# Kernel optimization log

Hardware: AMD Instinct MI355X
Metric: run time of the kernel (lower is better)

The kernel has to match this reference:

```python
import jax, jax.numpy as jnp
import numpy as np

WS = 8; SHIFT = 4; HEADS = 6
B = 2; H0 = 256; W0 = 256; C0 = 192; HID = 768; RED = 8


def _rel_pos_index(ws):
    coords = np.stack(np.meshgrid(np.arange(ws), np.arange(ws), indexing='ij')).reshape(2, -1)
    rel = (coords[:, :, None] - coords[:, None, :]).transpose(1, 2, 0)
    rel[:, :, 0] += ws - 1
    rel[:, :, 1] += ws - 1
    rel[:, :, 0] *= 2 * ws - 1
    return rel.sum(-1)  # (N, N) int


def _attn_mask(H, W, ws, shift):
    # exact translation of SwinTransformerBlock.calculate_mask (static, numpy)
    img = np.zeros((H, W))
    sl = (slice(0, -ws), slice(-ws, -shift), slice(-shift, None))
    cnt = 0
    for hs in sl:
        for wsl in sl:
            img[hs, wsl] = cnt
            cnt += 1
    mw = img.reshape(H // ws, ws, W // ws, ws).transpose(0, 2, 1, 3).reshape(-1, ws * ws)
    am = mw[:, None, :] - mw[:, :, None]  # (nW, N, N)
    return jnp.asarray(np.where(am != 0, -100.0, 0.0).astype(np.float32))


def _ln(x, g, b, eps=1e-5):
    m = x.mean(-1, keepdims=True)
    v = ((x - m) ** 2).mean(-1, keepdims=True)
    return (x - m) * jax.lax.rsqrt(v + eps) * g + b


def setup_inputs():
    key = jax.random.key(0)
    ks = jax.random.split(key, 12)
    C = C0
    r = C // RED
    def nrm(k, shape, std=0.02):
        return jax.random.normal(k, shape, dtype=jnp.float32) * std
    return {
        'x': jax.random.normal(ks[0], (B, H0 * W0, C), dtype=jnp.float32),
        'norm1_g': jnp.ones((C,), jnp.float32),
        'norm1_b': jnp.zeros((C,), jnp.float32),
        'qkv_w': nrm(ks[1], (3 * C, C)),
        'qkv_b': jnp.zeros((3 * C,), jnp.float32),
        'rpb_table': nrm(ks[2], ((2 * WS - 1) ** 2, HEADS)),
        'proj_w': nrm(ks[3], (C, C)),
        'proj_b': jnp.zeros((C,), jnp.float32),
        'norm2_g': jnp.ones((C,), jnp.float32),
        'norm2_b': jnp.zeros((C,), jnp.float32),
        'fc1_w': nrm(ks[4], (HID, C)),
        'fc1_b': jnp.zeros((HID,), jnp.float32),
        'fc2_w': nrm(ks[5], (C, HID)),
        'fc2_b': jnp.zeros((C,), jnp.float32),
        'lce_c1_w': nrm(ks[6], (r, C, 1, 1)),
        'lce_c1_b': jnp.zeros((r,), jnp.float32),
        'lce_c2_w': nrm(ks[7], (r, r, 3, 3)),
        'lce_c2_b': jnp.zeros((r,), jnp.float32),
        'lce_c3_w': nrm(ks[8], (C, r, 1, 1)),
        'lce_c3_b': jnp.zeros((C,), jnp.float32),
        'lce_fc1_w': nrm(ks[9], (r, C)),
        'lce_fc2_w': nrm(ks[10], (C, r)),
        'H': H0,
        'W': W0,
    }


def reference(x, norm1_g, norm1_b, qkv_w, qkv_b, rpb_table, proj_w, proj_b,
              norm2_g, norm2_b, fc1_w, fc1_b, fc2_w, fc2_b,
              lce_c1_w, lce_c1_b, lce_c2_w, lce_c2_b, lce_c3_w, lce_c3_b,
              lce_fc1_w, lce_fc2_w, H, W):
    Bs, L, C = x.shape
    ws, shift, nh = WS, SHIFT, HEADS
    hd = C // nh
    N = ws * ws
    shortcut = x
    xn = _ln(x, norm1_g, norm1_b).reshape(Bs, H, W, C)
    lcf = xn.transpose(0, 3, 1, 2)  # (B, C, H, W) local-context input
    # cyclic shift + window partition
    sx = jnp.roll(xn, (-shift, -shift), axis=(1, 2))
    nWh, nWw = H // ws, W // ws
    xw = sx.reshape(Bs, nWh, ws, nWw, ws, C).transpose(0, 1, 3, 2, 4, 5).reshape(-1, N, C)
    Bn = xw.shape[0]
    # W-MSA with relative position bias
    qkv = (xw @ qkv_w.T + qkv_b).reshape(Bn, N, 3, nh, hd).transpose(2, 0, 3, 1, 4)
    q, k, v = qkv[0], qkv[1], qkv[2]
    attn = jnp.einsum('bhnd,bhmd->bhnm', q * (hd ** -0.5), k)
    rpi = _rel_pos_index(ws)
    bias = rpb_table[rpi.reshape(-1)].reshape(N, N, nh).transpose(2, 0, 1)  # (nh, N, N)
    attn = attn + bias[None]
    mask = _attn_mask(H, W, ws, shift)  # (nW, N, N)
    nW = mask.shape[0]
    attn = (attn.reshape(Bs, nW, nh, N, N) + mask[None, :, None]).reshape(Bn, nh, N, N)
    attn = jax.nn.softmax(attn, axis=-1)
    out = jnp.einsum('bhnm,bhmd->bhnd', attn, v).transpose(0, 2, 1, 3).reshape(Bn, N, C)
    out = out @ proj_w.T + proj_b
    # window reverse + reverse shift
    sx = out.reshape(Bs, nWh, nWw, ws, ws, C).transpose(0, 1, 3, 2, 4, 5).reshape(Bs, H, W, C)
    xa = jnp.roll(sx, (shift, shift), axis=(1, 2)).reshape(Bs, H * W, C)
    x1 = shortcut + xa
    # MLP (exact GELU, matches torch default)
    h = _ln(x1, norm2_g, norm2_b)
    h = jax.nn.gelu(h @ fc1_w.T + fc1_b, approximate=False)
    x2 = x1 + (h @ fc2_w.T + fc2_b)
    # LocalContextExtractor: conv1x1 -> conv3x3 -> conv1x1 -> LeakyReLU(0.2) -> SE gate
    dn = ('NCHW', 'OIHW', 'NCHW')
    y = jax.lax.conv_general_dilated(lcf, lce_c1_w, (1, 1), 'VALID', dimension_numbers=dn) + lce_c1_b[None, :, None, None]
    y = jax.lax.conv_general_dilated(y, lce_c2_w, (1, 1), [(1, 1), (1, 1)], dimension_numbers=dn) + lce_c2_b[None, :, None, None]
    y = jax.lax.conv_general_dilated(y, lce_c3_w, (1, 1), 'VALID', dimension_numbers=dn) + lce_c3_b[None, :, None, None]
    y = jnp.where(y >= 0, y, 0.2 * y)
    s = y.mean((2, 3))  # (B, C) global avg pool
    s = jax.nn.sigmoid(jax.nn.relu(s @ lce_fc1_w.T) @ lce_fc2_w.T)
    lc = y * s[:, :, None, None]
    lc = lc.reshape(Bs, C, H * W).transpose(0, 2, 1)
    return lc + x2
```

## Files before the change

### kernel.cpp

```cpp
#include <hip/hip_runtime.h>
#include <hip/hip_bf16.h>

using bf16 = __hip_bfloat16;
typedef __attribute__((ext_vector_type(8))) short short8;
typedef __attribute__((ext_vector_type(4))) float float4v;

constexpr int NTOK = 131072;

constexpr size_t OFF_T1   = 50331648;
constexpr size_t OFF_T2   = 62914560;
constexpr size_t OFF_S0   = 75497472;
constexpr size_t OFF_WQKV = 75500544;
constexpr size_t OFF_WPRJ = 75721728;
constexpr size_t OFF_WFC1 = 75795456;
constexpr size_t OFF_WFC2 = 76090368;
constexpr size_t OFF_C1WB = 76385280;
constexpr size_t WS_NEEDED = 76397568;

__device__ __forceinline__ int region256(int t) { return t < 248 ? 0 : (t < 252 ? 1 : 2); }

__device__ __forceinline__ short8 lds8(const bf16* p) {
  return *reinterpret_cast<const short8*>(p);
}
__device__ __forceinline__ short8 glb8(const bf16* p) {
  return *reinterpret_cast<const short8*>(p);
}

__global__ __launch_bounds__(256) void k_f2b_all(const float* __restrict__ qkvw, const float* __restrict__ projw,
                                                 const float* __restrict__ w1, const float* __restrict__ w2,
                                                 const float* __restrict__ c1w,
                                                 bf16* __restrict__ wqkv, bf16* __restrict__ wprj,
                                                 bf16* __restrict__ wfc1, bf16* __restrict__ wfc2,
                                                 bf16* __restrict__ c1wb, float* __restrict__ s0) {
  int i = blockIdx.x * 256 + threadIdx.x;
  if (i < 110592) { wqkv[i] = __float2bfloat16(qkvw[i]); return; }
  i -= 110592;
  if (i < 36864) { wprj[i] = __float2bfloat16(projw[i]); return; }
  i -= 36864;
  if (i < 147456) { wfc1[i] = __float2bfloat16(w1[i]); return; }
  i -= 147456;
  if (i < 147456) { wfc2[i] = __float2bfloat16(w2[i]); return; }
  i -= 147456;
  if (i < 4608) { c1wb[i] = __float2bfloat16(c1w[i]); return; }
  i -= 4608;
  if (i < 1536) { c1wb[4608 + i] = __float2bfloat16(0.f); return; }
  i -= 1536;
  if (i < 384) s0[i] = 0.f;
}

__device__ __forceinline__ int stg_b(int r, int c) { return (r * 384 + c * 2) ^ ((r & 7) << 4); }
__device__ __forceinline__ int kl1_b(int r, int c) { return 24576 + ((r * 64 + c * 2) ^ ((r & 7) << 4)); }
__device__ __forceinline__ int vt1_b(int r, int c) { return 28672 + ((r * 128 + c * 2) ^ ((r & 7) << 4)); }
__device__ __forceinline__ int ps3_b(int r, int c) { return 32768 + ((r * 128 + c * 2) ^ ((r & 7) << 4)); }

__device__ __forceinline__ short8 lds8o(const char* sm, int byteoff) {
  return *reinterpret_cast<const short8*>(sm + byteoff);
}
__device__ __forceinline__ void st16(char* sm, int byteoff, bf16 v) {
  *reinterpret_cast<bf16*>(sm + byteoff) = v;
}

__global__ __launch_bounds__(256, 3) void k_attn2(const float* __restrict__ x, const float* __restrict__ g,
                                                  const float* __restrict__ bb, const bf16* __restrict__ wq,
                                                  const float* __restrict__ qkvb, const float* __restrict__ rpb,
                                                  const bf16* __restrict__ wp, const float* __restrict__ projb,
                                                  const bf16* __restrict__ c1wb, const float* __restrict__ c1b,
                                                  float* __restrict__ t1, float* __restrict__ x1out) {
  __shared__ char sm[40960];

  int win = blockIdx.x;
  int b = win >> 10;
  int wrem = win & 1023;
  int wh = wrem >> 5, ww = wrem & 31;
  int tid = threadIdx.x;
  int wave = tid >> 6, lane = tid & 63;
  int colB = lane & 15, grp = lane >> 4;
  const float scale = 0.17677669529663687f;

  for (int t = 0; t < 16; ++t) {
    int tok = wave * 16 + t;
    int i = tok >> 3, j = tok & 7;
    int hp = (wh * 8 + i + 4) & 255;
    int wpp = (ww * 8 + j + 4) & 255;
    const float* xr = x + (((size_t)b << 16) + (hp << 8) + wpp) * 192;
    float v0 = xr[lane], v1 = xr[lane + 64], v2 = xr[lane + 128];
    float s = v0 + v1 + v2;
    for (int o = 32; o > 0; o >>= 1) s += __shfl_down(s, o);
    s = __shfl(s, 0);
    float m = s * (1.f / 192.f);
    float d0 = v0 - m, d1 = v1 - m, d2 = v2 - m;
    float q = d0 * d0 + d1 * d1 + d2 * d2;
    for (int o = 32; o > 0; o >>= 1) q += __shfl_down(q, o);
    q = __shfl(q, 0);
    float inv = rsqrtf(q * (1.f / 192.f) + 1e-5f);
    st16(sm, stg_b(tok, lane),       __float2bfloat16(d0 * inv * g[lane]       + bb[lane]));
    st16(sm, stg_b(tok, lane + 64),  __float2bfloat16(d1 * inv * g[lane + 64]  + bb[lane + 64]));
    st16(sm, stg_b(tok, lane + 128), __float2bfloat16(d2 * inv * g[lane + 128] + bb[lane + 128]));
  }

  short8 axw[6];
#pragma unroll
  for (int kk = 0; kk < 6; ++kk) axw[kk] = lds8o(sm, stg_b(wave * 16 + colB, kk * 32 + 8 * grp));

  int l1r[4], i1r[4], j1r[4];
#pragma unroll
  for (int r = 0; r < 4; ++r) {
    int n = wave * 16 + 4 * grp + r;
    i1r[r] = n >> 3; j1r[r] = n & 7;
    l1r[r] = region256(wh * 8 + i1r[r]) * 3 + region256(ww * 8 + j1r[r]);
  }

  for (int gch = 0; gch < 6; ++gch) {
    float qreg[8];
    {
      float4v qa[2] = {{0,0,0,0},{0,0,0,0}};
      short8 wf[6];
#pragma unroll
      for (int h2 = 0; h2 < 2; ++h2) {
#pragma unroll
        for (int kk = 0; kk < 3; ++kk)
#pragma unroll
          for (int jt = 0; jt < 2; ++jt)
            wf[kk * 2 + jt] = glb8(wq + (size_t)(gch * 32 + jt * 16 + colB) * 192 + (h2 * 3 + kk) * 32 + 8 * grp);
#pragma unroll
        for (int kk = 0; kk < 3; ++kk)
#pragma unroll
          for (int jt = 0; jt < 2; ++jt)
            qa[jt] = __builtin_amdgcn_mfma_f32_16x16x32_bf16(axw[h2 * 3 + kk], wf[kk * 2 + jt], qa[jt], 0, 0, 0);
      }
#pragma unroll
      for (int jt = 0; jt < 2; ++jt) {
        float bias = qkvb[gch * 32 + jt * 16 + colB];
#pragma unroll
        for (int r = 0; r < 4; ++r) qreg[jt * 4 + r] = (qa[jt][r] + bias) * scale;
      }
    }
    {
      float4v ka[2] = {{0,0,0,0},{0,0,0,0}};
      short8 wf[6];
#pragma unroll
      for (int h2 = 0; h2 < 2; ++h2) {
#pragma unroll
        for (int kk = 0; kk < 3; ++kk)
#pragma unroll
          for (int jt = 0; jt < 2; ++jt)
            wf[kk * 2 + jt] = glb8(wq + (size_t)(192 + gch * 32 + jt * 16 + colB) * 192 + (h2 * 3 + kk) * 32 + 8 * grp);
#pragma unroll
        for (int kk = 0; kk < 3; ++kk)
#pragma unroll
          for (int jt = 0; jt < 2; ++jt)
            ka[jt] = __builtin_amdgcn_mfma_f32_16x16x32_bf16(axw[h2 * 3 + kk], wf[kk * 2 + jt], ka[jt], 0, 0, 0);
      }
#pragma unroll
      for (int jt = 0; jt < 2; ++jt) {
        float bias = qkvb[192 + gch * 32 + jt * 16 + colB];
#pragma unroll
        for (int r = 0; r < 4; ++r)
          st16(sm, kl1_b(wave * 16 + 4 * grp + r, jt * 16 + colB), __float2bfloat16(ka[jt][r] + bias));
      }
    }
    {
      float4v va[2] = {{0,0,0,0},{0,0,0,0}};
      short8 wf[6];
#pragma unroll
      for (int h2 = 0; h2 < 2; ++h2) {
#pragma unroll
        for (int kk = 0; kk < 3; ++kk)
#pragma unroll
          for (int jt = 0; jt < 2; ++jt)
            wf[kk * 2 + jt] = glb8(wq + (size_t)(384 + gch * 32 + jt * 16 + colB) * 192 + (h2 * 3 + kk) * 32 + 8 * grp);
#pragma unroll
        for (int kk = 0; kk < 3; ++kk)
#pragma unroll
          for (int jt = 0; jt < 2; ++jt)
            va[jt] = __builtin_amdgcn_mfma_f32_16x16x32_bf16(axw[h2 * 3 + kk], wf[kk * 2 + jt], va[jt], 0, 0, 0);
      }
#pragma unroll
      for (int jt = 0; jt < 2; ++jt) {
        float bias = qkvb[384 + gch * 32 + jt * 16 + colB];
#pragma unroll
        for (int r = 0; r < 4; ++r)
          st16(sm, vt1_b(jt * 16 + colB, wave * 16 + 4 * grp + r), __float2bfloat16(va[jt][r] + bias));
      }
    }
    if (gch == 0) {
      float4v acc[2] = {{0,0,0,0},{0,0,0,0}};
      short8 wf[6];
#pragma unroll
      for (int h2 = 0; h2 < 2; ++h2) {
#pragma unroll
        for (int kk = 0; kk < 3; ++kk)
#pragma unroll
          for (int j = 0; j < 2; ++j)
            wf[kk * 2 + j] = glb8(c1wb + (size_t)(j * 16 + colB) * 192 + (h2 * 3 + kk) * 32 + 8 * grp);
#pragma unroll
        for (int kk = 0; kk < 3; ++kk)
#pragma unroll
          for (int j = 0; j < 2; ++j)
            acc[j] = __builtin_amdgcn_mfma_f32_16x16x32_bf16(axw[h2 * 3 + kk], wf[kk * 2 + j], acc[j], 0, 0, 0);
      }
#pragma unroll
      for (int j = 0; j < 2; ++j) {
        int ch = j * 16 + colB;
        if (ch < 24) {
          float bias = c1b[ch];
#pragma unroll
          for (int r = 0; r < 4; ++r) {
            int tok = wave * 16 + 4 * grp + r;
            int i = tok >> 3, jj = tok & 7;
            int hp = (wh * 8 + i + 4) & 255;
            int wpp = (ww * 8 + jj + 4) & 255;
            size_t pix = ((size_t)b << 16) + (hp << 8) + wpp;
            t1[pix * 24 + ch] = acc[j][r] + bias;
          }
        }
      }
    }
    __syncthreads();

    {
      int h = gch;
#pragma unroll
      for (int t = 0; t < 2; ++t)
#pragma unroll
        for (int r = 0; r < 4; ++r)
          st16(sm, ps3_b(wave * 16 + 4 * grp + r, t * 16 + colB), __float2bfloat16(qreg[t * 4 + r]));
      short8 aq = lds8o(sm, ps3_b(wave * 16 + colB, 8 * grp));

      float4v s[4];
#pragma unroll
      for (int nt = 0; nt < 4; ++nt) {
        short8 bk = lds8o(sm, kl1_b(nt * 16 + colB, 8 * grp));
        float4v z = {0, 0, 0, 0};
        s[nt] = __builtin_amdgcn_mfma_f32_16x16x32_bf16(aq, bk, z, 0, 0, 0);
      }
#pragma unroll
      for (int nt = 0; nt < 4; ++nt) {
        int m = nt * 16 + colB;
        int i2 = m >> 3, j2 = m & 7;
        int l2 = region256(wh * 8 + i2) * 3 + region256(ww * 8 + j2);
#pragma unroll
        for (int r = 0; r < 4; ++r) {
          float bias = rpb[((i1r[r] - i2 + 7) * 15 + (j1r[r] - j2 + 7)) * 6 + h];
          s[nt][r] += bias + (l1r[r] != l2 ? -100.f : 0.f);
        }
      }
#pragma unroll
      for (int r = 0; r < 4; ++r) {
        float mx = fmaxf(fmaxf(s[0][r], s[1][r]), fmaxf(s[2][r], s[3][r]));
        mx = fmaxf(mx, __shfl_xor(mx, 1));
        mx = fmaxf(mx, __shfl_xor(mx, 2));
        mx = fmaxf(mx, __shfl_xor(mx, 4));
        mx = fmaxf(mx, __shfl_xor(mx, 8));
        float e0 = __expf(s[0][r] - mx), e1 = __expf(s[1][r] - mx);
        float e2 = __expf(s[2][r] - mx), e3 = __expf(s[3][r] - mx);
        float sum = e0 + e1 + e2 + e3;
        sum += __shfl_xor(sum, 1);
        sum += __shfl_xor(sum, 2);
        sum += __shfl_xor(sum, 4);
        sum += __shfl_xor(sum, 8);
        float inv = 1.f / sum;
        int row = wave * 16 + 4 * grp + r;
        st16(sm, ps3_b(row, 0 * 16 + colB), __float2bfloat16(e0 * inv));
        st16(sm, ps3_b(row, 1 * 16 + colB), __float2bfloat16(e1 * inv));
        st16(sm, ps3_b(row, 2 * 16 + colB), __float2bfloat16(e2 * inv));
        st16(sm, ps3_b(row, 3 * 16 + colB), __float2bfloat16(e3 * inv));
      }
      short8 ap0 = lds8o(sm, ps3_b(wave * 16 + colB, 8 * grp));
      short8 ap1 = lds8o(sm, ps3_b(wave * 16 + colB, 32 + 8 * grp));

      float4v o0 = {0, 0, 0, 0}, o1 = {0, 0, 0, 0};
      o0 = __builtin_amdgcn_mfma_f32_16x16x32_bf16(ap0, lds8o(sm, vt1_b(colB, 8 * grp)), o0, 0, 0, 0);
      o0 = __builtin_amdgcn_mfma_f32_16x16x32_bf16(ap1, lds8o(sm, vt1_b(colB, 32 + 8 * grp)), o0, 0, 0, 0);
      o1 = __builtin_amdgcn_mfma_f32_16x16x32_bf16(ap0, lds8o(sm, vt1_b(16 + colB, 8 * grp)), o1, 0, 0, 0);
      o1 = __builtin_amdgcn_mfma_f32_16x16x32_bf16(ap1, lds8o(sm, vt1_b(16 + colB, 32 + 8 * grp)), o1, 0, 0, 0);
      int ocol = gch * 32;
#pragma unroll
      for (int r = 0; r < 4; ++r) {
        int row = wave * 16 + 4 * grp + r;
        st16(sm, stg_b(row, ocol + colB),      __float2bfloat16(o0[r]));
        st16(sm, stg_b(row, ocol + 16 + colB), __float2bfloat16(o1[r]));
      }
    }
    if (gch != 5) __syncthreads();
  }

  short8 ao[6];
#pragma unroll
  for (int kk = 0; kk < 6; ++kk) ao[kk] = lds8o(sm, stg_b(wave * 16 + colB, kk * 32 + 8 * grp));
  for (int gp = 0; gp < 4; ++gp) {
    float4v acc[3] = {{0,0,0,0},{0,0,0,0},{0,0,0,0}};
#pragma unroll
    for (int half = 0; half < 2; ++half) {
      short8 wfp[9];
#pragma unroll
      for (int kk = 0; kk < 3; ++kk)
#pragma unroll
        for (int j = 0; j < 3; ++j)
          wfp[kk * 3 + j] = glb8(wp + (size_t)((gp * 3 + j) * 16 + colB) * 192 + (half * 3 + kk) * 32 + 8 * grp);
#pragma unroll
      for (int kk = 0; kk < 3; ++kk)
#pragma unroll
        for (int j = 0; j < 3; ++j)
          acc[j] = __builtin_amdgcn_mfma_f32_16x16x32_bf16(ao[half * 3 + kk], wfp[kk * 3 + j], acc[j], 0, 0, 0);
    }
#pragma unroll
    for (int j = 0; j < 3; ++j) {
      int col = (gp * 3 + j) * 16 + colB;
      float bias = projb[col];
#pragma unroll
      for (int r = 0; r < 4; ++r) {
        int n = wave * 16 + 4 * grp + r;
        int i = n >> 3, jj = n & 7;
        int hd2 = (wh * 8 + i + 4) & 255;
        int wd2 = (ww * 8 + jj + 4) & 255;
        size_t p = (((size_t)b << 16) + (hd2 << 8) + wd2) * 192 + col;
        x1out[p] = x[p] + acc[j][r] + bias;
      }
    }
  }
}

__global__ __launch_bounds__(256, 2) void k_mlp_lce2(float* __restrict__ x1, const float* __restrict__ g,
                                                     const float* __restrict__ bb, const bf16* __restrict__ w1,
                                                     const float* __restrict__ b1, const bf16* __restrict__ w2,
                                                     const float* __restrict__ b2,
                                                     const float* __restrict__ t1, const float* __restrict__ cw,
                                                     const float* __restrict__ cbia, float* __restrict__ t2,
                                                     const float* __restrict__ c3w, const float* __restrict__ c3b,
                                                     float* __restrict__ s0) {
  extern __shared__ __align__(16) char smu[];
  int tid = threadIdx.x;

  if (blockIdx.x < 512) {
    float* halo = (float*)smu;
    float* wlds = (float*)(smu + 32400);
    int bid = blockIdx.x;
    int b = bid >> 8;
    int rem = bid & 255;
    int ty0 = ((rem >> 4) & 15) * 16, tx0 = (rem & 15) * 16;
    for (int idx = tid; idx < 5184; idx += 256) wlds[idx] = cw[idx];
    for (int idx = tid; idx < 18 * 18 * 24; idx += 256) {
      int ch = idx % 24;
      int pp = idx / 24;
      int hy = pp / 18, hx = pp - hy * 18;
      int gy = ty0 + hy - 1, gx = tx0 + hx - 1;
      float v = 0.f;
      if (gy >= 0 && gy < 256 && gx >= 0 && gx < 256)
        v = t1[((size_t)(b << 16) + (gy << 8) + gx) * 24 + ch];
      halo[pp * 25 + ch] = v;
    }
    __syncthreads();
    int py = tid >> 4, px = tid & 15;
    float acc[24];
#pragma unroll
    for (int ro = 0; ro < 24; ++ro) acc[ro] = cbia[ro];
    for (int ky = 0; ky < 3; ++ky) {
      for (int kx = 0; kx < 3; ++kx) {
        int base = ((py + ky) * 18 + px + kx) * 25;
        float inb[24];
#pragma unroll
        for (int ri = 0; ri < 24; ++ri) inb[ri] = halo[base + ri];
        int wo = ky * 3 + kx;
#pragma unroll
        for (int ro = 0; ro < 24; ++ro) {
          float a = acc[ro];
#pragma unroll
          for (int ri = 0; ri < 24; ++ri) a += inb[ri] * wlds[ro * 216 + ri * 9 + wo];
          acc[ro] = a;
        }
      }
    }
    size_t pix = (size_t)(b << 16) + ((ty0 + py) << 8) + tx0 + px;
#pragma unroll
    for (int ro = 0; ro < 24; ++ro) t2[pix * 24 + ro] = acc[ro];

    __syncthreads();
    float* t2l = (float*)smu;
#pragma unroll
    for (int ro = 0; ro < 24; ++ro) t2l[tid * 28 + ro] = acc[ro];
    __syncthreads();
    if (tid < 192) {
      float wr3[24];
#pragma unroll
      for (int i2 = 0; i2 < 24; ++i2) wr3[i2] = c3w[tid * 24 + i2];
      float b3 = c3b[tid];
      float ps = 0.f;
      for (int p = 0; p < 256; ++p) {
        const float4v* rp = reinterpret_cast<const float4v*>(&t2l[p * 28]);
        float a = b3;
#pragma unroll
        for (int v = 0; v < 6; ++v) {
          float4v q = rp[v];
          a += q[0] * wr3[v * 4] + q[1] * wr3[v * 4 + 1] + q[2] * wr3[v * 4 + 2] + q[3] * wr3[v * 4 + 3];
        }
        ps += (a < 0.f) ? 0.2f * a : a;
      }
      atomicAdd(&s0[b * 192 + tid], ps);
    }
    return;
  }

  bf16 (*xl)[200] = reinterpret_cast<bf16(*)[200]>(smu);
  bf16 (*hh)[392] = reinterpret_cast<bf16(*)[392]>(smu + 25600);
  int wave = tid >> 6, lane = tid & 63;
  int colB = lane & 15, grp = lane >> 4;
  size_t tokbase = (size_t)(blockIdx.x - 512) * 64;

  for (int t = wave; t < 64; t += 4) {
    const float* xr = x1 + (tokbase + t) * 192;
    float v0 = xr[lane], v1 = xr[lane + 64], v2 = xr[lane + 128];
    float s = v0 + v1 + v2;
    for (int o = 32; o > 0; o >>= 1) s += __shfl_down(s, o);
    s = __shfl(s, 0);
    float m = s * (1.f / 192.f);
    float d0 = v0 - m, d1 = v1 - m, d2 = v2 - m;
    float qq = d0 * d0 + d1 * d1 + d2 * d2;
    for (int o = 32; o > 0; o >>= 1) qq += __shfl_down(qq, o);
    qq = __shfl(qq, 0);
    float inv = rsqrtf(qq * (1.f / 192.f) + 1e-5f);
    xl[t][lane]       = __float2bfloat16(d0 * inv * g[lane]       + bb[lane]);
    xl[t][lane + 64]  = __float2bfloat16(d1 * inv * g[lane + 64]  + bb[lane + 64]);
    xl[t][lane + 128] = __float2bfloat16(d2 * inv * g[lane + 128] + bb[lane + 128]);
  }
  __syncthreads();

  short8 a1f[6][2];
#pragma unroll
  for (int kk = 0; kk < 6; ++kk) {
    a1f[kk][0] = lds8(&xl[colB][kk * 32 + 8 * grp]);
    a1f[kk][1] = lds8(&xl[16 + colB][kk * 32 + 8 * grp]);
  }

  float4v d[3][4];
#pragma unroll
  for (int j = 0; j < 3; ++j)
#pragma unroll
    for (int tt = 0; tt < 4; ++tt) d[j][tt] = (float4v){0, 0, 0, 0};
  int ntb = wave * 3;

  for (int ph = 0; ph < 2; ++ph) {
    if (ph) __syncthreads();
    for (int nn = 0; nn < 6; ++nn) {
      int ntl = wave * 6 + nn;
      int colg = ph * 384 + ntl * 16 + colB;
      short8 wf1[6];
#pragma unroll
      for (int kk = 0; kk < 6; ++kk)
        wf1[kk] = glb8(w1 + (size_t)colg * 192 + kk * 32 + 8 * grp);
      float4v c0 = {0,0,0,0}, c1 = {0,0,0,0}, c2 = {0,0,0,0}, c3 = {0,0,0,0};
#pragma unroll
      for (int kk = 0; kk < 6; ++kk) {
        c0 = __builtin_amdgcn_mfma_f32_16x16x32_bf16(a1f[kk][0], wf1[kk], c0, 0, 0, 0);
        c1 = __builtin_amdgcn_mfma_f32_16x16x32_bf16(a1f[kk][1], wf1[kk], c1, 0, 0, 0);
        c2 = __builtin_amdgcn_mfma_f32_16x16x32_bf16(lds8(&xl[32 + colB][kk * 32 + 8 * grp]), wf1[kk], c2, 0, 0, 0);
        c3 = __builtin_amdgcn_mfma_f32_16x16x32_bf16(lds8(&xl[48 + colB][kk * 32 + 8 * grp]), wf1[kk], c3, 0, 0, 0);
      }
      float bias = b1[colg];
      int coll = ntl * 16 + colB;
#pragma unroll
      for (int r = 0; r < 4; ++r) {
        float v0 = c0[r] + bias;
        float v1 = c1[r] + bias;
        float v2 = c2[r] + bias;
        float v3 = c3[r] + bias;
        v0 = v0 * 0.5f * (1.f + erff(v0 * 0.70710678118654752f));
        v1 = v1 * 0.5f * (1.f + erff(v1 * 0.70710678118654752f));
        v2 = v2 * 0.5f * (1.f + erff(v2 * 0.70710678118654752f));
        v3 = v3 * 0.5f * (1.f + erff(v3 * 0.70710678118654752f));
        hh[4 * grp + r][coll]      = __float2bfloat16(v0);
        hh[16 + 4 * grp + r][coll] = __float2bfloat16(v1);
        hh[32 + 4 * grp + r][coll] = __float2bfloat16(v2);
        hh[48 + 4 * grp + r][coll] = __float2bfloat16(v3);
      }
    }
    __syncthreads();
    for (int kk = 0; kk < 12; ++kk) {
      int kol = kk * 32 + 8 * grp;
      int kog = ph * 384 + kol;
      short8 wf2[3];
#pragma unroll
      for (int j = 0; j < 3; ++j)
        wf2[j] = glb8(w2 + (size_t)((ntb + j) * 16 + colB) * 768 + kog);
      short8 h0 = lds8(&hh[colB][kol]);
      short8 h1 = lds8(&hh[16 + colB][kol]);
      short8 h2 = lds8(&hh[32 + colB][kol]);
      short8 h3 = lds8(&hh[48 + colB][kol]);
#pragma unroll
      for (int j = 0; j < 3; ++j) {
        d[j][0] = __builtin_amdgcn_mfma_f32_16x16x32_bf16(h0, wf2[j], d[j][0], 0, 0, 0);
        d[j][1] = __builtin_amdgcn_mfma_f32_16x16x32_bf16(h1, wf2[j], d[j][1], 0, 0, 0);
        d[j][2] = __builtin_amdgcn_mfma_f32_16x16x32_bf16(h2, wf2[j], d[j][2], 0, 0, 0);
        d[j][3] = __builtin_amdgcn_mfma_f32_16x16x32_bf16(h3, wf2[j], d[j][3], 0, 0, 0);
      }
    }
  }

#pragma unroll
  for (int j = 0; j < 3; ++j) {
    int col = (ntb + j) * 16 + colB;
    float bias = b2[col];
#pragma unroll
    for (int tt = 0; tt < 4; ++tt) {
#pragma unroll
      for (int r = 0; r < 4; ++r) {
        size_t p = (tokbase + tt * 16 + 4 * grp + r) * 192 + col;
        x1[p] += d[j][tt][r] + bias;
      }
    }
  }
}

__global__ __launch_bounds__(192) void k_final3(float* __restrict__ out, const float* __restrict__ t2,
                                                const float* __restrict__ c3w, const float* __restrict__ c3b,
                                                const float* __restrict__ s0, const float* __restrict__ w1se,
                                                const float* __restrict__ w2se) {
  __shared__ float mean[192];
  __shared__ float tt[24];
  __shared__ __align__(16) float t2l[64 * 24];
  int b = blockIdx.x >> 10;
  int chunk = blockIdx.x & 1023;
  int tid = threadIdx.x;
  mean[tid] = s0[b * 192 + tid] * (1.f / 65536.f);
  size_t pix0 = (size_t)b * 65536 + chunk * 64;
  for (int idx = tid; idx < 1536; idx += 192) t2l[idx] = t2[pix0 * 24 + idx];
  __syncthreads();
  if (tid < 24) {
    float a = 0.f;
    for (int c = 0; c < 192; ++c) a += mean[c] * w1se[tid * 192 + c];
    tt[tid] = fmaxf(a, 0.f);
  }
  __syncthreads();
  float a = 0.f;
#pragma unroll
  for (int r = 0; r < 24; ++r) a += tt[r] * w2se[tid * 24 + r];
  float gate = 1.f / (1.f + expf(-a));

  float wr3[24];
#pragma unroll
  for (int i = 0; i < 24; ++i) wr3[i] = c3w[tid * 24 + i];
  float b3 = c3b[tid];
  for (int p = 0; p < 64; ++p) {
    const float4v* rp = reinterpret_cast<const float4v*>(&t2l[p * 24]);
    float acc = b3;
#pragma unroll
    for (int v = 0; v < 6; ++v) {
      float4v q = rp[v];
      acc += q[0] * wr3[v * 4] + q[1] * wr3[v * 4 + 1] + q[2] * wr3[v * 4 + 2] + q[3] * wr3[v * 4 + 3];
    }
    if (acc < 0.f) acc *= 0.2f;
    out[(pix0 + p) * 192 + tid] += acc * gate;
  }
}

extern "C" void kernel_launch(void* const* d_in, const int* in_sizes, int n_in,
                              void* d_out, int out_size, void* d_ws, size_t ws_size,
                              hipStream_t stream) {
  const float* x     = (const float*)d_in[0];
  const float* n1g   = (const float*)d_in[1];
  const float* n1b   = (const float*)d_in[2];
  const float* qkvw  = (const float*)d_in[3];
  const float* qkvb  = (const float*)d_in[4];
  const float* rpb   = (const float*)d_in[5];
  const float* projw = (const float*)d_in[6];
  const float* projb = (const float*)d_in[7];
  const float* n2g   = (const float*)d_in[8];
  const float* n2b   = (const float*)d_in[9];
  const float* w1    = (const float*)d_in[10];
  const float* b1    = (const float*)d_in[11];
  const float* w2    = (const float*)d_in[12];
  const float* b2    = (const float*)d_in[13];
  const float* c1w   = (const float*)d_in[14];
  const float* c1b   = (const float*)d_in[15];
  const float* c2w   = (const float*)d_in[16];
  const float* c2b   = (const float*)d_in[17];
  const float* c3w   = (const float*)d_in[18];
  const float* c3b   = (const float*)d_in[19];
  const float* sfc1  = (const float*)d_in[20];
  const float* sfc2  = (const float*)d_in[21];
  float* out = (float*)d_out;

  if (ws_size < WS_NEEDED) return;

  char* ws = (char*)d_ws;
  float* t1   = (float*)(ws + OFF_T1);
  float* t2   = (float*)(ws + OFF_T2);
  float* s0   = (float*)(ws + OFF_S0);
  bf16*  wqkv = (bf16*)(ws + OFF_WQKV);
  bf16*  wprj = (bf16*)(ws + OFF_WPRJ);
  bf16*  wfc1 = (bf16*)(ws + OFF_WFC1);
  bf16*  wfc2 = (bf16*)(ws + OFF_WFC2);
  bf16*  c1wb = (bf16*)(ws + OFF_C1WB);

  hipFuncSetAttribute((const void*)k_mlp_lce2, hipFuncAttributeMaxDynamicSharedMemorySize, 75776);

  k_f2b_all<<<1754, 256, 0, stream>>>(qkvw, projw, w1, w2, c1w,
                                      wqkv, wprj, wfc1, wfc2, c1wb, s0);

  k_attn2<<<2048, 256, 0, stream>>>(x, n1g, n1b, wqkv, qkvb, rpb, wprj, projb,
                                    c1wb, c1b, t1, out);
  k_mlp_lce2<<<2560, 256, 75776, stream>>>(out, n2g, n2b, wfc1, b1, wfc2, b2,
                                           t1, c2w, c2b, t2, c3w, c3b, s0);
  k_final3<<<2048, 192, 0, stream>>>(out, t2, c3w, c3b, s0, sfc1, sfc2);
}
```

Baseline: 885.2 us.

## Process two adjacent windows per attention block to reuse weight fragments

```diff
diff --git a/kernel.cpp b/kernel.cpp
--- a/kernel.cpp
+++ b/kernel.cpp
@@ -49,9 +49,9 @@
 }
 
 __device__ __forceinline__ int stg_b(int r, int c) { return (r * 384 + c * 2) ^ ((r & 7) << 4); }
-__device__ __forceinline__ int kl1_b(int r, int c) { return 24576 + ((r * 64 + c * 2) ^ ((r & 7) << 4)); }
-__device__ __forceinline__ int vt1_b(int r, int c) { return 28672 + ((r * 128 + c * 2) ^ ((r & 7) << 4)); }
-__device__ __forceinline__ int ps3_b(int r, int c) { return 32768 + ((r * 128 + c * 2) ^ ((r & 7) << 4)); }
+__device__ __forceinline__ int kl1_b(int r, int c) { return 49152 + ((r * 64 + c * 2) ^ ((r & 7) << 4)); }
+__device__ __forceinline__ int vt1_b(int r, int c) { return 57344 + ((r * 256 + c * 2) ^ ((r & 7) << 4)); }
+__device__ __forceinline__ int ps3_b(int r, int c) { return 65536 + ((r * 128 + c * 2) ^ ((r & 7) << 4)); }
 
 __device__ __forceinline__ short8 lds8o(const char* sm, int byteoff) {
   return *reinterpret_cast<const short8*>(sm + byteoff);
@@ -60,60 +60,73 @@
   *reinterpret_cast<bf16*>(sm + byteoff) = v;
 }
 
-__global__ __launch_bounds__(256, 3) void k_attn2(const float* __restrict__ x, const float* __restrict__ g,
+constexpr int SMEM_ATTN = 73728;
+
+__global__ __launch_bounds__(256, 2) void k_attn2(const float* __restrict__ x, const float* __restrict__ g,
                                                   const float* __restrict__ bb, const bf16* __restrict__ wq,
                                                   const float* __restrict__ qkvb, const float* __restrict__ rpb,
                                                   const bf16* __restrict__ wp, const float* __restrict__ projb,
                                                   const bf16* __restrict__ c1wb, const float* __restrict__ c1b,
                                                   float* __restrict__ t1, float* __restrict__ x1out) {
-  __shared__ char sm[40960];
-
-  int win = blockIdx.x;
-  int b = win >> 10;
-  int wrem = win & 1023;
-  int wh = wrem >> 5, ww = wrem & 31;
+  extern __shared__ char sm[];
+
+  int pb = blockIdx.x;
+  int b = pb >> 9;
+  int rem = pb & 511;
+  int wh = rem >> 4, pw = rem & 15;
+  int ww0 = pw << 1;
   int tid = threadIdx.x;
   int wave = tid >> 6, lane = tid & 63;
   int colB = lane & 15, grp = lane >> 4;
   const float scale = 0.17677669529663687f;
 
-  for (int t = 0; t < 16; ++t) {
-    int tok = wave * 16 + t;
-    int i = tok >> 3, j = tok & 7;
-    int hp = (wh * 8 + i + 4) & 255;
-    int wpp = (ww * 8 + j + 4) & 255;
-    const float* xr = x + (((size_t)b << 16) + (hp << 8) + wpp) * 192;
-    float v0 = xr[lane], v1 = xr[lane + 64], v2 = xr[lane + 128];
-    float s = v0 + v1 + v2;
-    for (int o = 32; o > 0; o >>= 1) s += __shfl_down(s, o);
-    s = __shfl(s, 0);
-    float m = s * (1.f / 192.f);
-    float d0 = v0 - m, d1 = v1 - m, d2 = v2 - m;
-    float q = d0 * d0 + d1 * d1 + d2 * d2;
-    for (int o = 32; o > 0; o >>= 1) q += __shfl_down(q, o);
-    q = __shfl(q, 0);
-    float inv = rsqrtf(q * (1.f / 192.f) + 1e-5f);
-    st16(sm, stg_b(tok, lane),       __float2bfloat16(d0 * inv * g[lane]       + bb[lane]));
-    st16(sm, stg_b(tok, lane + 64),  __float2bfloat16(d1 * inv * g[lane + 64]  + bb[lane + 64]));
-    st16(sm, stg_b(tok, lane + 128), __float2bfloat16(d2 * inv * g[lane + 128] + bb[lane + 128]));
-  }
-
-  short8 axw[6];
-#pragma unroll
-  for (int kk = 0; kk < 6; ++kk) axw[kk] = lds8o(sm, stg_b(wave * 16 + colB, kk * 32 + 8 * grp));
-
-  int l1r[4], i1r[4], j1r[4];
+#pragma unroll
+  for (int wn = 0; wn < 2; ++wn) {
+    int wwc = ww0 + wn;
+    for (int t = 0; t < 16; ++t) {
+      int tok = wave * 16 + t;
+      int i = tok >> 3, j = tok & 7;
+      int hp = (wh * 8 + i + 4) & 255;
+      int wpp = (wwc * 8 + j + 4) & 255;
+      const float* xr = x + (((size_t)b << 16) + (hp << 8) + wpp) * 192;
+      float v0 = xr[lane], v1 = xr[lane + 64], v2 = xr[lane + 128];
+      float s = v0 + v1 + v2;
+      for (int o = 32; o > 0; o >>= 1) s += __shfl_down(s, o);
+      s = __shfl(s, 0);
+      float m = s * (1.f / 192.f);
+      float d0 = v0 - m, d1 = v1 - m, d2 = v2 - m;
+      float q = d0 * d0 + d1 * d1 + d2 * d2;
+      for (int o = 32; o > 0; o >>= 1) q += __shfl_down(q, o);
+      q = __shfl(q, 0);
+      float inv = rsqrtf(q * (1.f / 192.f) + 1e-5f);
+      int sr = wn * 64 + tok;
+      st16(sm, stg_b(sr, lane),       __float2bfloat16(d0 * inv * g[lane]       + bb[lane]));
+      st16(sm, stg_b(sr, lane + 64),  __float2bfloat16(d1 * inv * g[lane + 64]  + bb[lane + 64]));
+      st16(sm, stg_b(sr, lane + 128), __float2bfloat16(d2 * inv * g[lane + 128] + bb[lane + 128]));
+    }
+  }
+
+  short8 axwA[6], axwB[6];
+#pragma unroll
+  for (int kk = 0; kk < 6; ++kk) {
+    axwA[kk] = lds8o(sm, stg_b(wave * 16 + colB, kk * 32 + 8 * grp));
+    axwB[kk] = lds8o(sm, stg_b(64 + wave * 16 + colB, kk * 32 + 8 * grp));
+  }
+
+  int i1r[4], j1r[4], l1rA[4], l1rB[4];
 #pragma unroll
   for (int r = 0; r < 4; ++r) {
     int n = wave * 16 + 4 * grp + r;
     i1r[r] = n >> 3; j1r[r] = n & 7;
-    l1r[r] = region256(wh * 8 + i1r[r]) * 3 + region256(ww * 8 + j1r[r]);
+    int rh = region256(wh * 8 + i1r[r]) * 3;
+    l1rA[r] = rh + region256(ww0 * 8 + j1r[r]);
+    l1rB[r] = rh + region256((ww0 + 1) * 8 + j1r[r]);
   }
 
   for (int gch = 0; gch < 6; ++gch) {
-    float qreg[8];
+    float qreg[16];
     {
-      float4v qa[2] = {{0,0,0,0},{0,0,0,0}};
+      float4v qa[4] = {{0,0,0,0},{0,0,0,0},{0,0,0,0},{0,0,0,0}};
       short8 wf[6];
 #pragma unroll
       for (int h2 = 0; h2 < 2; ++h2) {
@@ -125,18 +138,23 @@
 #pragma unroll
         for (int kk = 0; kk < 3; ++kk)
 #pragma unroll
-          for (int jt = 0; jt < 2; ++jt)
-            qa[jt] = __builtin_amdgcn_mfma_f32_16x16x32_bf16(axw[h2 * 3 + kk], wf[kk * 2 + jt], qa[jt], 0, 0, 0);
+          for (int jt = 0; jt < 2; ++jt) {
+            qa[jt]     = __builtin_amdgcn_mfma_f32_16x16x32_bf16(axwA[h2 * 3 + kk], wf[kk * 2 + jt], qa[jt], 0, 0, 0);
+            qa[2 + jt] = __builtin_amdgcn_mfma_f32_16x16x32_bf16(axwB[h2 * 3 + kk], wf[kk * 2 + jt], qa[2 + jt], 0, 0, 0);
+          }
       }
 #pragma unroll
       for (int jt = 0; jt < 2; ++jt) {
         float bias = qkvb[gch * 32 + jt * 16 + colB];
 #pragma unroll
-        for (int r = 0; r < 4; ++r) qreg[jt * 4 + r] = (qa[jt][r] + bias) * scale;
+        for (int r = 0; r < 4; ++r) {
+          qreg[jt * 4 + r]     = (qa[jt][r] + bias) * scale;
+          qreg[8 + jt * 4 + r] = (qa[2 + jt][r] + bias) * scale;
+        }
       }
     }
     {
-      float4v ka[2] = {{0,0,0,0},{0,0,0,0}};
+      float4v ka[4] = {{0,0,0,0},{0,0,0,0},{0,0,0,0},{0,0,0,0}};
       short8 wf[6];
 #pragma unroll
       for (int h2 = 0; h2 < 2; ++h2) {
@@ -148,19 +166,23 @@
 #pragma unroll
         for (int kk = 0; kk < 3; ++kk)
 #pragma unroll
-          for (int jt = 0; jt < 2; ++jt)
-            ka[jt] = __builtin_amdgcn_mfma_f32_16x16x32_bf16(axw[h2 * 3 + kk], wf[kk * 2 + jt], ka[jt], 0, 0, 0);
+          for (int jt = 0; jt < 2; ++jt) {
+            ka[jt]     = __builtin_amdgcn_mfma_f32_16x16x32_bf16(axwA[h2 * 3 + kk], wf[kk * 2 + jt], ka[jt], 0, 0, 0);
+            ka[2 + jt] = __builtin_amdgcn_mfma_f32_16x16x32_bf16(axwB[h2 * 3 + kk], wf[kk * 2 + jt], ka[2 + jt], 0, 0, 0);
+          }
       }
 #pragma unroll
       for (int jt = 0; jt < 2; ++jt) {
         float bias = qkvb[192 + gch * 32 + jt * 16 + colB];
 #pragma unroll
-        for (int r = 0; r < 4; ++r)
+        for (int r = 0; r < 4; ++r) {
           st16(sm, kl1_b(wave * 16 + 4 * grp + r, jt * 16 + colB), __float2bfloat16(ka[jt][r] + bias));
+          st16(sm, kl1_b(64 + wave * 16 + 4 * grp + r, jt * 16 + colB), __float2bfloat16(ka[2 + jt][r] + bias));
+        }
       }
     }
     {
-      float4v va[2] = {{0,0,0,0},{0,0,0,0}};
+      float4v va[4] = {{0,0,0,0},{0,0,0,0},{0,0,0,0},{0,0,0,0}};
       short8 wf[6];
 #pragma unroll
       for (int h2 = 0; h2 < 2; ++h2) {
@@ -172,19 +194,24 @@
 #pragma unroll
         for (int kk = 0; kk < 3; ++kk)
 #pragma unroll
-          for (int jt = 0; jt < 2; ++jt)
-            va[jt] = __builtin_amdgcn_mfma_f32_16x16x32_bf16(axw[h2 * 3 + kk], wf[kk * 2 + jt], va[jt], 0, 0, 0);
+          for (int jt = 0; jt < 2; ++jt) {
+            va[jt]     = __builtin_amdgcn_mfma_f32_16x16x32_bf16(axwA[h2 * 3 + kk], wf[kk * 2 + jt], va[jt], 0, 0, 0);
+            va[2 + jt] = __builtin_amdgcn_mfma_f32_16x16x32_bf16(axwB[h2 * 3 + kk], wf[kk * 2 + jt], va[2 + jt], 0, 0, 0);
+          }
       }
 #pragma unroll
       for (int jt = 0; jt < 2; ++jt) {
         float bias = qkvb[384 + gch * 32 + jt * 16 + colB];
 #pragma unroll
-        for (int r = 0; r < 4; ++r)
+        for (int r = 0; r < 4; ++r) {
           st16(sm, vt1_b(jt * 16 + colB, wave * 16 + 4 * grp + r), __float2bfloat16(va[jt][r] + bias));
+          st16(sm, vt1_b(jt * 16 + colB, 64 + wave * 16 + 4 * grp + r), __float2bfloat16(va[2 + jt][r] + bias));
+        }
       }
     }
     if (gch == 0) {
-      float4v acc[2] = {{0,0,0,0},{0,0,0,0}};
+      float4v accA[2] = {{0,0,0,0},{0,0,0,0}};
+      float4v accB[2] = {{0,0,0,0},{0,0,0,0}};
       short8 wf[6];
 #pragma unroll
       for (int h2 = 0; h2 < 2; ++h2) {
@@ -196,8 +223,10 @@
 #pragma unroll
         for (int kk = 0; kk < 3; ++kk)
 #pragma unroll
-          for (int j = 0; j < 2; ++j)
-            acc[j] = __builtin_amdgcn_mfma_f32_16x16x32_bf16(axw[h2 * 3 + kk], wf[kk * 2 + j], acc[j], 0, 0, 0);
+          for (int j = 0; j < 2; ++j) {
+            accA[j] = __builtin_amdgcn_mfma_f32_16x16x32_bf16(axwA[h2 * 3 + kk], wf[kk * 2 + j], accA[j], 0, 0, 0);
+            accB[j] = __builtin_amdgcn_mfma_f32_16x16x32_bf16(axwB[h2 * 3 + kk], wf[kk * 2 + j], accB[j], 0, 0, 0);
+          }
       }
 #pragma unroll
       for (int j = 0; j < 2; ++j) {
@@ -209,28 +238,31 @@
             int tok = wave * 16 + 4 * grp + r;
             int i = tok >> 3, jj = tok & 7;
             int hp = (wh * 8 + i + 4) & 255;
-            int wpp = (ww * 8 + jj + 4) & 255;
-            size_t pix = ((size_t)b << 16) + (hp << 8) + wpp;
-            t1[pix * 24 + ch] = acc[j][r] + bias;
+            int wppA = (ww0 * 8 + jj + 4) & 255;
+            int wppB = ((ww0 + 1) * 8 + jj + 4) & 255;
+            t1[(((size_t)b << 16) + (hp << 8) + wppA) * 24 + ch] = accA[j][r] + bias;
+            t1[(((size_t)b << 16) + (hp << 8) + wppB) * 24 + ch] = accB[j][r] + bias;
           }
         }
       }
     }
     __syncthreads();
 
-    {
+#pragma unroll
+    for (int wn = 0; wn < 2; ++wn) {
       int h = gch;
+      int wwc = ww0 + wn;
 #pragma unroll
       for (int t = 0; t < 2; ++t)
 #pragma unroll
         for (int r = 0; r < 4; ++r)
-          st16(sm, ps3_b(wave * 16 + 4 * grp + r, t * 16 + colB), __float2bfloat16(qreg[t * 4 + r]));
+          st16(sm, ps3_b(wave * 16 + 4 * grp + r, t * 16 + colB), __float2bfloat16(qreg[wn * 8 + t * 4 + r]));
       short8 aq = lds8o(sm, ps3_b(wave * 16 + colB, 8 * grp));
 
       float4v s[4];
 #pragma unroll
       for (int nt = 0; nt < 4; ++nt) {
-        short8 bk = lds8o(sm, kl1_b(nt * 16 + colB, 8 * grp));
+        short8 bk = lds8o(sm, kl1_b(wn * 64 + nt * 16 + colB, 8 * grp));
         float4v z = {0, 0, 0, 0};
         s[nt] = __builtin_amdgcn_mfma_f32_16x16x32_bf16(aq, bk, z, 0, 0, 0);
       }
@@ -238,11 +270,12 @@
       for (int nt = 0; nt < 4; ++nt) {
         int m = nt * 16 + colB;
         int i2 = m >> 3, j2 = m & 7;
-        int l2 = region256(wh * 8 + i2) * 3 + region256(ww * 8 + j2);
+        int l2 = region256(wh * 8 + i2) * 3 + region256(wwc * 8 + j2);
 #pragma unroll
         for (int r = 0; r < 4; ++r) {
+          int l1 = wn ? l1rB[r] : l1rA[r];
           float bias = rpb[((i1r[r] - i2 + 7) * 15 + (j1r[r] - j2 + 7)) * 6 + h];
-          s[nt][r] += bias + (l1r[r] != l2 ? -100.f : 0.f);
+          s[nt][r] += bias + (l1 != l2 ? -100.f : 0.f);
         }
       }
 #pragma unroll
@@ -270,14 +303,14 @@
       short8 ap1 = lds8o(sm, ps3_b(wave * 16 + colB, 32 + 8 * grp));
 
       float4v o0 = {0, 0, 0, 0}, o1 = {0, 0, 0, 0};
-      o0 = __builtin_amdgcn_mfma_f32_16x16x32_bf16(ap0, lds8o(sm, vt1_b(colB, 8 * grp)), o0, 0, 0, 0);
-      o0 = __builtin_amdgcn_mfma_f32_16x16x32_bf16(ap1, lds8o(sm, vt1_b(colB, 32 + 8 * grp)), o0, 0, 0, 0);
-      o1 = __builtin_amdgcn_mfma_f32_16x16x32_bf16(ap0, lds8o(sm, vt1_b(16 + colB, 8 * grp)), o1, 0, 0, 0);
-      o1 = __builtin_amdgcn_mfma_f32_16x16x32_bf16(ap1, lds8o(sm, vt1_b(16 + colB, 32 + 8 * grp)), o1, 0, 0, 0);
+      o0 = __builtin_amdgcn_mfma_f32_16x16x32_bf16(ap0, lds8o(sm, vt1_b(colB, wn * 64 + 8 * grp)), o0, 0, 0, 0);
+      o0 = __builtin_amdgcn_mfma_f32_16x16x32_bf16(ap1, lds8o(sm, vt1_b(colB, wn * 64 + 32 + 8 * grp)), o0, 0, 0, 0);
+      o1 = __builtin_amdgcn_mfma_f32_16x16x32_bf16(ap0, lds8o(sm, vt1_b(16 + colB, wn * 64 + 8 * grp)), o1, 0, 0, 0);
+      o1 = __builtin_amdgcn_mfma_f32_16x16x32_bf16(ap1, lds8o(sm, vt1_b(16 + colB, wn * 64 + 32 + 8 * grp)), o1, 0, 0, 0);
       int ocol = gch * 32;
 #pragma unroll
       for (int r = 0; r < 4; ++r) {
-        int row = wave * 16 + 4 * grp + r;
+        int row = wn * 64 + wave * 16 + 4 * grp + r;
         st16(sm, stg_b(row, ocol + colB),      __float2bfloat16(o0[r]));
         st16(sm, stg_b(row, ocol + 16 + colB), __float2bfloat16(o1[r]));
       }
@@ -285,11 +318,15 @@
     if (gch != 5) __syncthreads();
   }
 
-  short8 ao[6];
-#pragma unroll
-  for (int kk = 0; kk < 6; ++kk) ao[kk] = lds8o(sm, stg_b(wave * 16 + colB, kk * 32 + 8 * grp));
+  short8 aoA[6], aoB[6];
+#pragma unroll
+  for (int kk = 0; kk < 6; ++kk) {
+    aoA[kk] = lds8o(sm, stg_b(wave * 16 + colB, kk * 32 + 8 * grp));
+    aoB[kk] = lds8o(sm, stg_b(64 + wave * 16 + colB, kk * 32 + 8 * grp));
+  }
   for (int gp = 0; gp < 4; ++gp) {
-    float4v acc[3] = {{0,0,0,0},{0,0,0,0},{0,0,0,0}};
+    float4v accA[3] = {{0,0,0,0},{0,0,0,0},{0,0,0,0}};
+    float4v accB[3] = {{0,0,0,0},{0,0,0,0},{0,0,0,0}};
 #pragma unroll
     for (int half = 0; half < 2; ++half) {
       short8 wfp[9];
@@ -301,8 +338,10 @@
 #pragma unroll
       for (int kk = 0; kk < 3; ++kk)
 #pragma unroll
-        for (int j = 0; j < 3; ++j)
-          acc[j] = __builtin_amdgcn_mfma_f32_16x16x32_bf16(ao[half * 3 + kk], wfp[kk * 3 + j], acc[j], 0, 0, 0);
+        for (int j = 0; j < 3; ++j) {
+          accA[j] = __builtin_amdgcn_mfma_f32_16x16x32_bf16(aoA[half * 3 + kk], wfp[kk * 3 + j], accA[j], 0, 0, 0);
+          accB[j] = __builtin_amdgcn_mfma_f32_16x16x32_bf16(aoB[half * 3 + kk], wfp[kk * 3 + j], accB[j], 0, 0, 0);
+        }
     }
 #pragma unroll
     for (int j = 0; j < 3; ++j) {
@@ -313,9 +352,12 @@
         int n = wave * 16 + 4 * grp + r;
         int i = n >> 3, jj = n & 7;
         int hd2 = (wh * 8 + i + 4) & 255;
-        int wd2 = (ww * 8 + jj + 4) & 255;
-        size_t p = (((size_t)b << 16) + (hd2 << 8) + wd2) * 192 + col;
-        x1out[p] = x[p] + acc[j][r] + bias;
+        int wdA = (ww0 * 8 + jj + 4) & 255;
+        int wdB = ((ww0 + 1) * 8 + jj + 4) & 255;
+        size_t pA = (((size_t)b << 16) + (hd2 << 8) + wdA) * 192 + col;
+        size_t pB = (((size_t)b << 16) + (hd2 << 8) + wdB) * 192 + col;
+        x1out[pA] = x[pA] + accA[j][r] + bias;
+        x1out[pB] = x[pB] + accB[j][r] + bias;
       }
     }
   }
@@ -592,13 +634,14 @@
   bf16*  wfc2 = (bf16*)(ws + OFF_WFC2);
   bf16*  c1wb = (bf16*)(ws + OFF_C1WB);
 
+  hipFuncSetAttribute((const void*)k_attn2, hipFuncAttributeMaxDynamicSharedMemorySize, SMEM_ATTN);
   hipFuncSetAttribute((const void*)k_mlp_lce2, hipFuncAttributeMaxDynamicSharedMemorySize, 75776);
 
   k_f2b_all<<<1754, 256, 0, stream>>>(qkvw, projw, w1, w2, c1w,
                                       wqkv, wprj, wfc1, wfc2, c1wb, s0);
 
-  k_attn2<<<2048, 256, 0, stream>>>(x, n1g, n1b, wqkv, qkvb, rpb, wprj, projb,
-                                    c1wb, c1b, t1, out);
+  k_attn2<<<1024, 256, SMEM_ATTN, stream>>>(x, n1g, n1b, wqkv, qkvb, rpb, wprj, projb,
+                                            c1wb, c1b, t1, out);
   k_mlp_lce2<<<2560, 256, 75776, stream>>>(out, n2g, n2b, wfc1, b1, wfc2, b2,
                                            t1, c2w, c2b, t2, c3w, c3b, s0);
   k_final3<<<2048, 192, 0, stream>>>(out, t2, c3w, c3b, s0, sfc1, sfc2);
```

Result: faster. 799.5 us (-9.7%).
